# Performance work log

Hardware: AMD Instinct MI355X
Metric: run time of the kernel (lower is better)

Reference implementation:

```python
import jax, jax.numpy as jnp
from jax import lax
import numpy as np

HID = 1000


def _lstm_cell(x, h, c, W_ih, W_hh, b_ih, b_hh):
    # PyTorch nn.LSTMCell gate order: i, f, g, o
    gates = x @ W_ih.T + b_ih + h @ W_hh.T + b_hh  # [B, 4H]
    i, f, g, o = jnp.split(gates, 4, axis=-1)
    c2 = jax.nn.sigmoid(f) * c + jax.nn.sigmoid(i) * jnp.tanh(g)
    h2 = jax.nn.sigmoid(o) * jnp.tanh(c2)
    return h2, c2


def setup_inputs() -> dict:
    key = jax.random.key(0)
    ks = jax.random.split(key, 8)
    B, T, nbones = 256, 49, 64
    D = nbones * 3
    s = 0.05
    inp = {"enc_in": jax.random.normal(ks[0], (B, T, D), jnp.float32)}
    dims = [D, HID, HID]
    for l in range(3):
        inp[f"W_ih{l}"] = jax.random.normal(ks[1 + 2 * l], (4 * HID, dims[l]), jnp.float32) * s
        inp[f"W_hh{l}"] = jax.random.normal(ks[2 + 2 * l], (4 * HID, HID), jnp.float32) * s
        inp[f"b_ih{l}"] = jnp.zeros((4 * HID,), jnp.float32)
        inp[f"b_hh{l}"] = jnp.zeros((4 * HID,), jnp.float32)
    inp["train"] = 0  # eval mode: dropout is identity
    return inp


def reference(enc_in, W_ih0, W_hh0, b_ih0, b_hh0,
              W_ih1, W_hh1, b_ih1, b_hh1,
              W_ih2, W_hh2, b_ih2, b_hh2, train):
    params = [(W_ih0, W_hh0, b_ih0, b_hh0),
              (W_ih1, W_hh1, b_ih1, b_hh1),
              (W_ih2, W_hh2, b_ih2, b_hh2)]
    B = enc_in.shape[0]
    zeros = jnp.zeros((B, HID), enc_in.dtype)
    init = (tuple(zeros for _ in range(3)), tuple(zeros for _ in range(3)))

    def step(carry, x):
        hs, cs = carry
        new_h, new_c = [], []
        inp = x
        for l in range(3):
            h2, c2 = _lstm_cell(inp, hs[l], cs[l], *params[l])
            new_h.append(h2)
            new_c.append(c2)
            inp = h2  # dropout with train=False is identity
        return (tuple(new_h), tuple(new_c)), jnp.stack(new_h)  # [3, B, H]

    # scan over time: enc_in [B, T, D] -> [T, B, D]
    _, ys = lax.scan(step, init, jnp.transpose(enc_in, (1, 0, 2)))
    # ys: [T, 3, B, H] -> [3, B, T, H]; equals the original per-layer `output`
    out = jnp.transpose(ys, (1, 2, 0, 3))
    return out
```

## Files before the change

### kernel.cpp

```cpp
#include <hip/hip_runtime.h>

#define HID_ 1000
#define NB 256
#define TT 49
#define DIN 192
#define NPAD 1024
#define M_ALL (TT * 256)

typedef _Float16 f16;
typedef _Float16 f16x4 __attribute__((ext_vector_type(4)));
typedef _Float16 f16x8 __attribute__((ext_vector_type(8)));
typedef float f32x4 __attribute__((ext_vector_type(4)));
typedef float f32x16 __attribute__((ext_vector_type(16)));
typedef const __attribute__((address_space(1))) unsigned int* gas_u32;
typedef __attribute__((address_space(3))) unsigned int* las_u32;

__device__ __forceinline__ float sigmf_(float x) {
    return 1.0f / (1.0f + __expf(-x));
}
__device__ __forceinline__ float tanhf_(float x) {
    float ax = fabsf(x);
    float e = __expf(-2.0f * ax);
    float t = (1.0f - e) / (1.0f + e);
    return copysignf(t, x);
}

__global__ __launch_bounds__(256) void conv_weight_v(
    const float* __restrict__ src, f16* __restrict__ dst, int K, int KPADv, int total8) {
    int idx = blockIdx.x * blockDim.x + threadIdx.x;
    if (idx >= total8) return;
    const int kpw = KPADv >> 3;
    const int kp = (idx % kpw) << 3;
    const int rest = idx / kpw;
    const int np = rest & 1023;
    const int g = rest >> 10;
    f16x8 v = {};
    if (np < HID_ && kp < K) {
        const float* sp = src + (size_t)(g * HID_ + np) * K + kp;
        float4 a = *(const float4*)sp;
        float4 b = *(const float4*)(sp + 4);
        v[0] = (f16)a.x; v[1] = (f16)a.y; v[2] = (f16)a.z; v[3] = (f16)a.w;
        v[4] = (f16)b.x; v[5] = (f16)b.y; v[6] = (f16)b.z; v[7] = (f16)b.w;
    }
    *(f16x8*)(dst + (size_t)rest * KPADv + kp) = v;
}

__global__ __launch_bounds__(256) void conv_x_v(
    const float* __restrict__ src, f16* __restrict__ dst, int total8) {
    int idx = blockIdx.x * blockDim.x + threadIdx.x;
    if (idx >= total8) return;
    const int kp = (idx % (DIN / 8)) << 3;
    const int rest = idx / (DIN / 8);
    const int b = rest & 255;
    const int t = rest >> 8;
    const float* sp = src + ((size_t)b * TT + t) * DIN + kp;
    float4 a = *(const float4*)sp;
    float4 c = *(const float4*)(sp + 4);
    f16x8 v;
    v[0] = (f16)a.x; v[1] = (f16)a.y; v[2] = (f16)a.z; v[3] = (f16)a.w;
    v[4] = (f16)c.x; v[5] = (f16)c.y; v[6] = (f16)c.z; v[7] = (f16)c.w;
    *(f16x8*)(dst + (size_t)rest * DIN + kp) = v;
}

__global__ void conv_bias(const float* __restrict__ bih, const float* __restrict__ bhh,
                          float* __restrict__ dst) {
    int idx = blockIdx.x * blockDim.x + threadIdx.x;
    if (idx < 4 * NPAD) {
        int np = idx & (NPAD - 1);
        int g = idx >> 10;
        float v = 0.0f;
        if (np < HID_) v = bih[g * HID_ + np] + bhh[g * HID_ + np];
        dst[idx] = v;
    }
}

__global__ __launch_bounds__(256) void input_gemm(
    const f16* __restrict__ A, int lda, int kiters,
    const f16* __restrict__ W, int ldw,
    const float* __restrict__ bias,
    f16* __restrict__ pre2) {
    __shared__ f16 As[128 * 64];
    __shared__ f16 Bs[128 * 64];
    const int id = blockIdx.x;
    const int sw = (id & 7) * (gridDim.x >> 3) + (id >> 3);
    const int m0 = (sw >> 5) << 7;
    const int n0 = (sw & 31) << 7;
    const int w = threadIdx.x >> 6;
    const int lane = threadIdx.x & 63;
    const int r = lane & 15;
    const int u = lane >> 4;
    const int kb8 = u << 3;
    const int wm = (w >> 1) << 6, wn = (w & 1) << 6;
    const int strow = (w << 5) + (lane >> 3);
    const int stcol = (lane & 7) << 3;

    f32x4 acc[4][4];
#pragma unroll
    for (int i = 0; i < 4; i++)
#pragma unroll
        for (int j = 0; j < 4; j++) acc[i][j] = (f32x4){0.f, 0.f, 0.f, 0.f};

    for (int kt = 0; kt < kiters; kt++) {
        const int k0 = kt << 6;
#pragma unroll
        for (int q = 0; q < 4; q++) {
            const int row = strow + (q << 3);
            const int cbase = ((w << 5) + (q << 3)) << 6;
            const f16* ga = A + (size_t)(m0 + row) * lda + k0 + stcol;
            const f16* gb = W + (size_t)(n0 + row) * ldw + k0 + stcol;
            __builtin_amdgcn_global_load_lds((gas_u32)ga, (las_u32)(As + cbase), 16, 0, 0);
            __builtin_amdgcn_global_load_lds((gas_u32)gb, (las_u32)(Bs + cbase), 16, 0, 0);
        }
        __syncthreads();
#pragma unroll
        for (int ks = 0; ks < 2; ks++) {
            f16x8 av[4], bv[4];
#pragma unroll
            for (int i = 0; i < 4; i++)
                av[i] = *(const f16x8*)(As + ((wm + i * 16 + r) << 6) + (ks << 5) + kb8);
#pragma unroll
            for (int j = 0; j < 4; j++)
                bv[j] = *(const f16x8*)(Bs + ((wn + j * 16 + r) << 6) + (ks << 5) + kb8);
#pragma unroll
            for (int i = 0; i < 4; i++)
#pragma unroll
                for (int j = 0; j < 4; j++)
                    acc[i][j] = __builtin_amdgcn_mfma_f32_16x16x32_f16(av[i], bv[j], acc[i][j], 0, 0, 0);
        }
        __syncthreads();
    }

#pragma unroll
    for (int j = 0; j < 4; j++) {
        const int gcol = n0 + wn + j * 16 + r;
        const float bj = bias[gcol];
        const int g = gcol >> 10;
        const int jt2 = (gcol & 1023) >> 5;
        const int col32 = gcol & 31;
#pragma unroll
        for (int i = 0; i < 4; i++) {
            const int grow = m0 + wm + i * 16 + (u << 2);
            const int t_ = grow >> 8;
            const int bt2 = (grow >> 5) & 7;
            const int lane2 = col32 + ((u & 1) << 5);
            const int regbase = ((i & 1) << 3) + ((u >> 1) << 2);
            f16x4 hv;
#pragma unroll
            for (int q = 0; q < 4; q++) hv[q] = (f16)(acc[i][j][q] + bj);
            *(f16x4*)(pre2 + ((((size_t)t_ * 8 + bt2) * 32 + jt2) * 4 + g) * 1024 +
                      lane2 * 16 + regbase) = hv;
        }
    }
}

__global__ __launch_bounds__(512, 2) void rec_persist(
    const f16* __restrict__ Whh, const f16* __restrict__ pre2,
    f16* __restrict__ hall, float* __restrict__ outl,
    unsigned int* __restrict__ flags) {
    __shared__ __align__(16) char smem[64 * 1024];
    __shared__ float pl[2 * 4 * 32 * 34];
    const int bid = blockIdx.x;
    const int bt = bid & 7;
    const int jt = bid >> 3;
    const int b0 = bt << 5;
    const int jc0 = jt << 5;
    const int tid = threadIdx.x;
    const int w = tid >> 6;
    const int g = w >> 1;
    const int kh = w & 1;
    const int lane = tid & 63;
    const int row = lane & 31;
    const int kg = lane >> 5;

    f16x8 wreg[32];
    {
        const f16* wp = Whh + ((size_t)(g * NPAD + jc0 + row)) * NPAD + (kh << 9) + (kg << 3);
#pragma unroll
        for (int ks = 0; ks < 32; ks++) wreg[ks] = *(const f16x8*)(wp + ks * 16);
    }

    const int eb = tid >> 4;
    const int ej = (tid & 15) << 1;
    float cv[2] = {0.f, 0.f};
    unsigned int* myflags = flags + bt * TT;
    const size_t preblk = ((((size_t)bt) * 32 + jt) * 4 + g) * 1024 + lane * 16;

    auto LOADP = [&](int tindex, f16x8& pa, f16x8& pb) {
        if (kh == 0) {
            const f16* pp = pre2 + (size_t)tindex * 8 * 32 * 4 * 1024 + preblk;
            pa = *(const f16x8*)pp;
            pb = *(const f16x8*)(pp + 8);
        }
    };

    auto STEP = [&](int t, f16x8& pc0, f16x8& pc1, f16x8& pn0, f16x8& pn1) {
        LOADP(t + 1 < TT ? t + 1 : t, pn0, pn1);

        if (t > 0) {
            while (__hip_atomic_load(myflags + (t - 1), __ATOMIC_RELAXED,
                                     __HIP_MEMORY_SCOPE_AGENT) < 32u) {}
            asm volatile("" ::: "memory");
            const f16* hread = hall + (size_t)(t - 1) * NB * NPAD;
#pragma unroll
            for (int i = 0; i < 8; i++) {
                int c = tid + (i << 9);
                int srow = c >> 7;
                int cb = (c & 127) << 4;
                f16x8 v = *(const f16x8*)(hread + (size_t)(b0 + srow) * NPAD + (cb >> 1));
                *(f16x8*)(smem + srow * 2048 + (cb ^ (srow << 4))) = v;
            }
        }
        __syncthreads();

        f32x16 acc;
#pragma unroll
        for (int reg = 0; reg < 16; reg++)
            acc[reg] = (kh == 0) ? (float)(reg < 8 ? pc0[reg] : pc1[reg - 8]) : 0.f;

        if (t > 0) {
#pragma unroll
            for (int ks = 0; ks < 32; ks++) {
                const int bc = (kh << 10) + ks * 32 + (kg << 4);
                f16x8 a = *(const f16x8*)(smem + row * 2048 + (bc ^ (row << 4)));
                acc = __builtin_amdgcn_mfma_f32_32x32x16_f16(a, wreg[ks], acc, 0, 0, 0);
            }
        }

#pragma unroll
        for (int reg = 0; reg < 16; reg++) {
            const int prow = (reg & 3) + ((reg >> 2) << 3) + (kg << 2);
            pl[((kh * 4 + g) * 32 + prow) * 34 + row] = acc[reg];
        }
        __syncthreads();

        float hvv[2];
        {
            float gv[4][2];
#pragma unroll
            for (int gate = 0; gate < 4; gate++) {
                float2 p0 = *(const float2*)&pl[((0 * 4 + gate) * 32 + eb) * 34 + ej];
                float2 p1 = *(const float2*)&pl[((1 * 4 + gate) * 32 + eb) * 34 + ej];
                gv[gate][0] = p0.x + p1.x;
                gv[gate][1] = p0.y + p1.y;
            }
#pragma unroll
            for (int q = 0; q < 2; q++) {
                float cn = sigmf_(gv[1][q]) * cv[q] + sigmf_(gv[0][q]) * tanhf_(gv[2][q]);
                hvv[q] = sigmf_(gv[3][q]) * tanhf_(cn);
                cv[q] = cn;
            }
        }
        {
            union { f16 h2[2]; unsigned uu; } cvt;
            cvt.h2[0] = (f16)hvv[0];
            cvt.h2[1] = (f16)hvv[1];
            __hip_atomic_store(
                (unsigned*)(hall + ((size_t)t * NB + b0 + eb) * NPAD + jc0 + ej), cvt.uu,
                __ATOMIC_RELAXED, __HIP_MEMORY_SCOPE_AGENT);
        }
        __syncthreads();
        if (tid == 0)
            __hip_atomic_fetch_add(myflags + t, 1u, __ATOMIC_RELAXED, __HIP_MEMORY_SCOPE_AGENT);
        const int col = jc0 + ej;
        if (col < HID_) {
            *(float2*)(outl + ((size_t)(b0 + eb) * TT + t) * HID_ + col) =
                make_float2(hvv[0], hvv[1]);
        }
    };

    f16x8 pA0 = {}, pA1 = {}, pB0 = {}, pB1 = {};
    LOADP(0, pA0, pA1);
    for (int t = 0; t < TT; t += 2) {
        STEP(t, pA0, pA1, pB0, pB1);
        if (t + 1 < TT) STEP(t + 1, pB0, pB1, pA0, pA1);
    }
}

extern "C" void kernel_launch(void* const* d_in, const int* in_sizes, int n_in,
                              void* d_out, int out_size, void* d_ws, size_t ws_size,
                              hipStream_t stream) {
    const float* enc_in = (const float*)d_in[0];
    const float* W_ih[3] = {(const float*)d_in[1], (const float*)d_in[5], (const float*)d_in[9]};
    const float* W_hh[3] = {(const float*)d_in[2], (const float*)d_in[6], (const float*)d_in[10]};
    const float* b_ih[3] = {(const float*)d_in[3], (const float*)d_in[7], (const float*)d_in[11]};
    const float* b_hh[3] = {(const float*)d_in[4], (const float*)d_in[8], (const float*)d_in[12]};
    float* out = (float*)d_out;

    char* ws = (char*)d_ws;
    size_t off = 0;
    auto alloc = [&](size_t bytes) {
        char* p = ws + off;
        off += (bytes + 255) & ~(size_t)255;
        return p;
    };
    f16* Wih_c[3];
    f16* Whh_c[3];
    Wih_c[0] = (f16*)alloc(4ull * NPAD * DIN * sizeof(f16));
    Whh_c[0] = (f16*)alloc(4ull * NPAD * NPAD * sizeof(f16));
    Wih_c[1] = (f16*)alloc(4ull * NPAD * NPAD * sizeof(f16));
    Whh_c[1] = (f16*)alloc(4ull * NPAD * NPAD * sizeof(f16));
    Wih_c[2] = (f16*)alloc(4ull * NPAD * NPAD * sizeof(f16));
    Whh_c[2] = (f16*)alloc(4ull * NPAD * NPAD * sizeof(f16));
    float* bias_c[3];
    for (int l = 0; l < 3; l++) bias_c[l] = (float*)alloc(4ull * NPAD * sizeof(float));
    f16* xbf = (f16*)alloc((size_t)TT * NB * DIN * sizeof(f16));
    f16* hall[3];
    for (int l = 0; l < 3; l++) hall[l] = (f16*)alloc((size_t)TT * NB * NPAD * sizeof(f16));
    f16* pre2 = (f16*)alloc((size_t)M_ALL * 4096 * sizeof(f16));
    unsigned int* flags = (unsigned int*)alloc(3ull * 8 * TT * sizeof(unsigned int));

    hipMemsetAsync(flags, 0, 3ull * 8 * TT * sizeof(unsigned int), stream);

    {
        int t8_l0 = 4 * NPAD * DIN / 8;
        conv_weight_v<<<(t8_l0 + 255) / 256, 256, 0, stream>>>(W_ih[0], Wih_c[0], DIN, DIN, t8_l0);
        int t8 = 4 * NPAD * NPAD / 8;
        conv_weight_v<<<(t8 + 255) / 256, 256, 0, stream>>>(W_hh[0], Whh_c[0], HID_, NPAD, t8);
        conv_weight_v<<<(t8 + 255) / 256, 256, 0, stream>>>(W_ih[1], Wih_c[1], HID_, NPAD, t8);
        conv_weight_v<<<(t8 + 255) / 256, 256, 0, stream>>>(W_hh[1], Whh_c[1], HID_, NPAD, t8);
        conv_weight_v<<<(t8 + 255) / 256, 256, 0, stream>>>(W_ih[2], Wih_c[2], HID_, NPAD, t8);
        conv_weight_v<<<(t8 + 255) / 256, 256, 0, stream>>>(W_hh[2], Whh_c[2], HID_, NPAD, t8);
    }
    {
        int t8x = TT * NB * (DIN / 8);
        conv_x_v<<<(t8x + 255) / 256, 256, 0, stream>>>(enc_in, xbf, t8x);
    }
    for (int l = 0; l < 3; l++)
        conv_bias<<<(4 * NPAD + 255) / 256, 256, 0, stream>>>(b_ih[l], b_hh[l], bias_c[l]);

    for (int l = 0; l < 3; l++) {
        if (l == 0)
            input_gemm<<<3136, 256, 0, stream>>>(xbf, DIN, DIN / 64, Wih_c[0], DIN,
                                                 bias_c[0], pre2);
        else
            input_gemm<<<3136, 256, 0, stream>>>(hall[l - 1], NPAD, NPAD / 64, Wih_c[l], NPAD,
                                                 bias_c[l], pre2);
        rec_persist<<<256, 512, 0, stream>>>(
            Whh_c[l], pre2, hall[l], out + (size_t)l * NB * TT * HID_,
            flags + (size_t)l * 8 * TT);
    }
}
```

Measured before the change: 1.079 ms.

## Replace input GEMM with 256x256-tile, 4-stage pipelined 8-wave kernel

```diff
diff --git a/kernel.cpp b/kernel.cpp
--- a/kernel.cpp
+++ b/kernel.cpp
@@ -74,80 +74,110 @@
     }
 }
 
-__global__ __launch_bounds__(256) void input_gemm(
-    const f16* __restrict__ A, int lda, int kiters,
+__global__ __launch_bounds__(512) void gemm8(
+    const f16* __restrict__ A, int lda, int nkt,
     const f16* __restrict__ W, int ldw,
     const float* __restrict__ bias,
     f16* __restrict__ pre2) {
-    __shared__ f16 As[128 * 64];
-    __shared__ f16 Bs[128 * 64];
+    __shared__ f16 lds[4][2][8192];
     const int id = blockIdx.x;
     const int sw = (id & 7) * (gridDim.x >> 3) + (id >> 3);
-    const int m0 = (sw >> 5) << 7;
-    const int n0 = (sw & 31) << 7;
-    const int w = threadIdx.x >> 6;
-    const int lane = threadIdx.x & 63;
-    const int r = lane & 15;
-    const int u = lane >> 4;
-    const int kb8 = u << 3;
-    const int wm = (w >> 1) << 6, wn = (w & 1) << 6;
-    const int strow = (w << 5) + (lane >> 3);
-    const int stcol = (lane & 7) << 3;
-
-    f32x4 acc[4][4];
-#pragma unroll
-    for (int i = 0; i < 4; i++)
-#pragma unroll
-        for (int j = 0; j < 4; j++) acc[i][j] = (f32x4){0.f, 0.f, 0.f, 0.f};
-
-    for (int kt = 0; kt < kiters; kt++) {
-        const int k0 = kt << 6;
-#pragma unroll
-        for (int q = 0; q < 4; q++) {
-            const int row = strow + (q << 3);
-            const int cbase = ((w << 5) + (q << 3)) << 6;
-            const f16* ga = A + (size_t)(m0 + row) * lda + k0 + stcol;
-            const f16* gb = W + (size_t)(n0 + row) * ldw + k0 + stcol;
-            __builtin_amdgcn_global_load_lds((gas_u32)ga, (las_u32)(As + cbase), 16, 0, 0);
-            __builtin_amdgcn_global_load_lds((gas_u32)gb, (las_u32)(Bs + cbase), 16, 0, 0);
-        }
-        __syncthreads();
-#pragma unroll
-        for (int ks = 0; ks < 2; ks++) {
-            f16x8 av[4], bv[4];
-#pragma unroll
-            for (int i = 0; i < 4; i++)
-                av[i] = *(const f16x8*)(As + ((wm + i * 16 + r) << 6) + (ks << 5) + kb8);
-#pragma unroll
-            for (int j = 0; j < 4; j++)
-                bv[j] = *(const f16x8*)(Bs + ((wn + j * 16 + r) << 6) + (ks << 5) + kb8);
-#pragma unroll
-            for (int i = 0; i < 4; i++)
-#pragma unroll
-                for (int j = 0; j < 4; j++)
-                    acc[i][j] = __builtin_amdgcn_mfma_f32_16x16x32_f16(av[i], bv[j], acc[i][j], 0, 0, 0);
-        }
-        __syncthreads();
-    }
-
-#pragma unroll
-    for (int j = 0; j < 4; j++) {
-        const int gcol = n0 + wn + j * 16 + r;
+    const int mt = sw >> 4;
+    const int nt = sw & 15;
+    const int m0 = mt << 8, n0 = nt << 8;
+    const int tid = threadIdx.x;
+    const int w = tid >> 6, lane = tid & 63;
+    const int r = lane & 15, u = lane >> 4;
+    const int wr = w >> 2, wc = w & 3;
+
+    const int srow = (w << 5) + (lane >> 2);
+    const int pslot = lane & 3;
+
+    f32x4 acc[8][4];
+#pragma unroll
+    for (int mf = 0; mf < 8; mf++)
+#pragma unroll
+        for (int nf = 0; nf < 4; nf++) acc[mf][nf] = (f32x4){0.f, 0.f, 0.f, 0.f};
+
+    auto STAGE = [&](int kt, int o) {
+        const int b = kt & 3;
+        const int row = srow + (o << 4);
+        const int ls = pslot ^ (row & 3);
+        const f16* ga = A + (size_t)(m0 + row) * lda + kt * 32 + ls * 8;
+        const f16* gb = W + (size_t)(n0 + row) * ldw + kt * 32 + ls * 8;
+        f16* da = &lds[b][0][0] + (w << 10) + (o << 9);
+        f16* db = &lds[b][1][0] + (w << 10) + (o << 9);
+        __builtin_amdgcn_global_load_lds((gas_u32)ga, (las_u32)da, 16, 0, 0);
+        __builtin_amdgcn_global_load_lds((gas_u32)gb, (las_u32)db, 16, 0, 0);
+    };
+    auto RDA = [&](int b, int fr) -> f16x8 {
+        const int row = (wr << 7) + fr * 16 + r;
+        return *(const f16x8*)(&lds[b][0][0] + row * 32 + ((u ^ (row & 3)) << 3));
+    };
+    auto RDB = [&](int b, int nf) -> f16x8 {
+        const int row = (wc << 6) + nf * 16 + r;
+        return *(const f16x8*)(&lds[b][1][0] + row * 32 + ((u ^ (row & 3)) << 3));
+    };
+
+    STAGE(0, 0); STAGE(0, 1); STAGE(1, 0); STAGE(1, 1);
+    asm volatile("s_waitcnt vmcnt(4)" ::: "memory");
+    __builtin_amdgcn_s_barrier();
+    __builtin_amdgcn_sched_barrier(0);
+
+    for (int kt = 0; kt < nkt; kt++) {
+        const int b = kt & 3;
+        const bool st = (kt + 2) < nkt;
+        f16x8 bv[4], av[4];
+#pragma unroll
+        for (int nf = 0; nf < 4; nf++) bv[nf] = RDB(b, nf);
+#pragma unroll
+        for (int mf = 0; mf < 4; mf++) av[mf] = RDA(b, mf);
+        if (st) STAGE(kt + 2, 0);
+        __builtin_amdgcn_s_barrier();
+        __builtin_amdgcn_s_setprio(1);
+#pragma unroll
+        for (int mf = 0; mf < 4; mf++)
+#pragma unroll
+            for (int nf = 0; nf < 4; nf++)
+                acc[mf][nf] = __builtin_amdgcn_mfma_f32_16x16x32_f16(
+                    av[mf], bv[nf], acc[mf][nf], 0, 0, 0);
+        __builtin_amdgcn_s_setprio(0);
+        __builtin_amdgcn_s_barrier();
+#pragma unroll
+        for (int mf = 0; mf < 4; mf++) av[mf] = RDA(b, 4 + mf);
+        if (st) STAGE(kt + 2, 1);
+        __builtin_amdgcn_s_barrier();
+        __builtin_amdgcn_s_setprio(1);
+#pragma unroll
+        for (int mf = 0; mf < 4; mf++)
+#pragma unroll
+            for (int nf = 0; nf < 4; nf++)
+                acc[4 + mf][nf] = __builtin_amdgcn_mfma_f32_16x16x32_f16(
+                    av[mf], bv[nf], acc[4 + mf][nf], 0, 0, 0);
+        __builtin_amdgcn_s_setprio(0);
+        if (st) asm volatile("s_waitcnt vmcnt(4)" ::: "memory");
+        else    asm volatile("s_waitcnt vmcnt(0)" ::: "memory");
+        __builtin_amdgcn_s_barrier();
+        __builtin_amdgcn_sched_barrier(0);
+    }
+
+#pragma unroll
+    for (int nf = 0; nf < 4; nf++) {
+        const int gcol = n0 + (wc << 6) + nf * 16 + r;
         const float bj = bias[gcol];
         const int g = gcol >> 10;
         const int jt2 = (gcol & 1023) >> 5;
         const int col32 = gcol & 31;
-#pragma unroll
-        for (int i = 0; i < 4; i++) {
-            const int grow = m0 + wm + i * 16 + (u << 2);
-            const int t_ = grow >> 8;
+        const int lane2 = col32 + ((u & 1) << 5);
+#pragma unroll
+        for (int mf = 0; mf < 8; mf++) {
+            const int grow = m0 + (wr << 7) + mf * 16 + (u << 2);
             const int bt2 = (grow >> 5) & 7;
-            const int lane2 = col32 + ((u & 1) << 5);
-            const int regbase = ((i & 1) << 3) + ((u >> 1) << 2);
+            const int regbase = ((mf & 1) << 3) + ((u >> 1) << 2);
             f16x4 hv;
 #pragma unroll
-            for (int q = 0; q < 4; q++) hv[q] = (f16)(acc[i][j][q] + bj);
-            *(f16x4*)(pre2 + ((((size_t)t_ * 8 + bt2) * 32 + jt2) * 4 + g) * 1024 +
+            for (int q = 0; q < 4; q++) hv[q] = (f16)(acc[mf][nf][q] + bj);
+            *(f16x4*)(pre2 + ((((size_t)mt * 8 + bt2) * 32 + jt2) * 4 + g) * 1024 +
                       lane2 * 16 + regbase) = hv;
         }
     }
@@ -330,11 +360,11 @@
 
     for (int l = 0; l < 3; l++) {
         if (l == 0)
-            input_gemm<<<3136, 256, 0, stream>>>(xbf, DIN, DIN / 64, Wih_c[0], DIN,
-                                                 bias_c[0], pre2);
+            gemm8<<<784, 512, 0, stream>>>(xbf, DIN, DIN / 32, Wih_c[0], DIN,
+                                           bias_c[0], pre2);
         else
-            input_gemm<<<3136, 256, 0, stream>>>(hall[l - 1], NPAD, NPAD / 64, Wih_c[l], NPAD,
-                                                 bias_c[l], pre2);
+            gemm8<<<784, 512, 0, stream>>>(hall[l - 1], NPAD, NPAD / 32, Wih_c[l], NPAD,
+                                           bias_c[l], pre2);
         rec_persist<<<256, 512, 0, stream>>>(
             Whh_c[l], pre2, hall[l], out + (size_t)l * NB * TT * HID_,
             flags + (size_t)l * 8 * TT);
```

Result: faster. 1.055 ms (median of 2 runs) (-2.2%).
